# Optimization experiments

Measured on AMD Instinct MI355X. Metric: run time of the kernel, lower is better.

## Reference

```python
import jax, jax.numpy as jnp
import numpy as np

NB = 10   # num_boxes
NC = 14   # num_classes
LC = 19   # channels per anchor: conf, x, y, w, h + NC classes
N_OBJ = 256


def _split(t):
    # t: [B, NB*LC, H, W] -> (conf, x, y, w, h), each [B, NB, H, W]
    return tuple(t[:, i:NB * LC + i:LC] for i in range(5))


def _iou_corners(b1, b2):
    # b1, b2: [..., 4] as (x1, y1, x2, y2)
    x1 = jnp.maximum(b1[..., 0], b2[..., 0])
    y1 = jnp.maximum(b1[..., 1], b2[..., 1])
    x2 = jnp.minimum(b1[..., 2], b2[..., 2])
    y2 = jnp.minimum(b1[..., 3], b2[..., 3])
    inter = jnp.clip(x2 - x1, 0.0) * jnp.clip(y2 - y1, 0.0)
    a1 = jnp.abs((b1[..., 2] - b1[..., 0]) * (b1[..., 3] - b1[..., 1]))
    a2 = jnp.abs((b2[..., 2] - b2[..., 0]) * (b2[..., 3] - b2[..., 1]))
    return inter / (a1 + a2 - inter + 1e-6)


def _responsible_anchor(pred_boxes, target_boxes, grids):
    # Faithful port of YOLOLoss.IOUcalc including its sequential integer state
    # and the quirky membership row max_IOU[b][:][h][w] == max_IOU[b, h, w, :].
    B, _, H, W, _ = pred_boxes.shape
    b, g, h, w = grids[:, 0], grids[:, 1], grids[:, 2], grids[:, 3]
    tb = target_boxes[b, g, h, w]                 # [N, 4]
    pb = pred_boxes[b, :, h, w]                   # [N, NB, 4]
    ious = jax.lax.stop_gradient(_iou_corners(tb[:, None, :], pb))  # [N, NB]
    maxI0 = jnp.zeros((B, NB, H, W), jnp.int32)

    def step(mI, inp):
        grid, iou_row = inp
        gb, gg, gh, gw = grid[0], grid[1], grid[2], grid[3]

        def anchor(a, mI):
            cur = mI[gb, gg, gh, gw]
            row = mI[gb, gh, gw, :]  # torch quirk: anchor dim indexed by h, H dim by w
            cond = (cur.astype(iou_row.dtype) < iou_row[a]) & jnp.all(row != a)
            return mI.at[gb, gg, gh, gw].set(jnp.where(cond, a, cur))

        return jax.lax.fori_loop(0, NB, anchor, mI), None

    maxI, _ = jax.lax.scan(step, maxI0, (grids, ious))
    return maxI


def _yolo_loss(predictions, targets, valid_grids,
               lambda_coord=5.0, lambda_noobj=5.0, lambda_loc=7.0):
    tc, tx, ty, tw, th = _split(targets)
    pc, px, py, pw, ph = _split(predictions)
    # corner-format boxes [B, NB, H, W, 4]
    pb = jnp.stack((px - pw / 2, py - ph / 2, px + pw / 2, py + ph / 2), -1)
    tb = jnp.stack((tx - tw / 2, ty - th / 2, tx + tw / 2, ty + th / 2), -1)
    maxI = _responsible_anchor(pb, tb, valid_grids)

    b, g, h, w = valid_grids[:, 0], valid_grids[:, 1], valid_grids[:, 2], valid_grids[:, 3]
    sel = maxI[b, g, h, w]       # responsible anchor for w/h/conf/class terms
    sel_xy = maxI[b, g, h, h]    # original bug: grids[2] used twice for x/y terms
    n = valid_grids.shape[0]

    x_l = (tx[b, g, h, w] - px[b, sel_xy, h, w]) ** 2
    y_l = (ty[b, g, h, w] - py[b, sel_xy, h, w]) ** 2
    w_l = (jnp.sqrt(jnp.clip(tw[b, g, h, w], 0.0)) - jnp.sqrt(jnp.clip(pw[b, sel, h, w], 0.0))) ** 2
    h_l = (jnp.sqrt(jnp.clip(th[b, g, h, w], 0.0)) - jnp.sqrt(jnp.clip(ph[b, sel, h, w], 0.0))) ** 2
    localization = jnp.sum(x_l + y_l + w_l + h_l) / n

    conf_obj = jnp.sum((tc[b, g, h, w] - pc[b, sel, h, w]) ** 2) / n

    conf_nothing = ((tc - pc) ** 2).at[b, sel, h, w].set(0.0).mean()

    cls_off = jnp.arange(NC)
    p_cls = predictions[b[:, None], (sel * LC + 5)[:, None] + cls_off, h[:, None], w[:, None]]  # [N, NC]
    t_cls = targets[b[:, None], (b * LC + 5)[:, None] + cls_off, h[:, None], w[:, None]]        # original bug: b*19
    class_loss = jnp.sum(jnp.mean((p_cls - t_cls) ** 2, axis=1)) / n

    return (lambda_loc * localization + lambda_coord * conf_obj
            + lambda_noobj * conf_nothing + class_loss)


def setup_inputs() -> dict:
    key = jax.random.key(0)
    B, H, W = 8, 96, 96
    C = NB * LC
    k1, k2, k3 = jax.random.split(key, 3)
    predictions = jax.random.uniform(k1, (B, C, H, W), jnp.float32)
    targets = jax.random.uniform(k2, (B, C, H, W), jnp.float32)
    targets = targets.at[:, 0:C:LC].set(0.0)  # confidence zero everywhere
    # 256 unique object cells; quirky-indexing constraints: b < 10, h < NB, H == W
    H_OBJ = 10
    rng = np.random.default_rng(0)
    flat = rng.choice(B * NB * H_OBJ * W, size=N_OBJ, replace=False)
    gb, r = np.divmod(flat, NB * H_OBJ * W)
    gg, r = np.divmod(r, H_OBJ * W)
    gh, gw = np.divmod(r, W)
    grids = np.stack([gb, gg, gh, gw], axis=1)
    grids = grids[np.lexsort((gw, gh, gg, gb))]  # torch.unique(dim=0) sorts rows
    valid_grids = jnp.asarray(grids, jnp.int32)
    conf = jax.random.uniform(k3, (N_OBJ,), jnp.float32, minval=0.3, maxval=1.0)
    targets = targets.at[valid_grids[:, 0], valid_grids[:, 1] * LC,
                         valid_grids[:, 2], valid_grids[:, 3]].set(conf)
    return {"predictions": predictions, "targets": targets, "valid_grids": valid_grids}


def reference(predictions, targets, valid_grids):
    return _yolo_loss(predictions, targets, valid_grids)
```

## Files before the change

kernel.cpp:

```cpp
#include <hip/hip_runtime.h>

#define NBANCH 10
#define NCLS   14
#define LCH    19
#define NOBJ   256
#define BBATCH 8
#define HH     96
#define WW     96
#define NCHTOT 190
#define PLANE  (HH*WW)
#define TOTCONF (BBATCH*NBANCH*PLANE)
#define NCONFBLK 720

__device__ __forceinline__ float ldat(const float* __restrict__ p, int b, int c, int hw) {
    return p[(size_t)(b * NCHTOT + c) * PLANE + hw];
}

#define IOU_OFF 0
#define XY_OFF  2560
#define WH_OFF  5120
#define CO_OFF  7680
#define CLS_OFF 10240
#define SUB_OFF 12800

__global__ __launch_bounds__(256) void fused_pre(const float* __restrict__ pred,
                                                 const float* __restrict__ targ,
                                                 const int* __restrict__ grids,
                                                 double* __restrict__ conf_part,
                                                 float* __restrict__ gw) {
    if (blockIdx.x < NCONFBLK) {
        int tid = blockIdx.x * 256 + threadIdx.x;
        int plane = tid / 2304;
        int r = tid - plane * 2304;
        int b = plane / NBANCH;
        int g = plane - b * NBANCH;
        size_t off = (size_t)(b * NCHTOT + g * LCH) * PLANE + (size_t)r * 4;
        float4 t4 = *reinterpret_cast<const float4*>(targ + off);
        float4 p4 = *reinterpret_cast<const float4*>(pred + off);
        float dx = t4.x - p4.x, dy = t4.y - p4.y, dz = t4.z - p4.z, dw = t4.w - p4.w;
        double s = (double)(dx*dx) + (double)(dy*dy) + (double)(dz*dz) + (double)(dw*dw);
        for (int o = 32; o > 0; o >>= 1) s += __shfl_down(s, o, 64);
        __shared__ double wsum[4];
        int lane = threadIdx.x & 63, wid = threadIdx.x >> 6;
        if (lane == 0) wsum[wid] = s;
        __syncthreads();
        if (threadIdx.x == 0) conf_part[blockIdx.x] = wsum[0] + wsum[1] + wsum[2] + wsum[3];
        return;
    }

    int gi = blockIdx.x - NCONFBLK;
    int a = threadIdx.x;
    if (a >= NBANCH) return;
    const int b = grids[gi*4+0], g = grids[gi*4+1], h = grids[gi*4+2], w = grids[gi*4+3];
    const int hw = h * WW + w;

    const float tc = ldat(targ, b, g*LCH+0, hw);
    const float tx = ldat(targ, b, g*LCH+1, hw);
    const float ty = ldat(targ, b, g*LCH+2, hw);
    const float tw = ldat(targ, b, g*LCH+3, hw);
    const float th = ldat(targ, b, g*LCH+4, hw);
    const float tb0 = tx - tw*0.5f, tb1 = ty - th*0.5f;
    const float tb2 = tx + tw*0.5f, tb3 = ty + th*0.5f;
    const float ta  = fabsf((tb2 - tb0) * (tb3 - tb1));

    const float pc = ldat(pred, b, a*LCH+0, hw);
    const float px = ldat(pred, b, a*LCH+1, hw);
    const float py = ldat(pred, b, a*LCH+2, hw);
    const float pw = ldat(pred, b, a*LCH+3, hw);
    const float ph = ldat(pred, b, a*LCH+4, hw);
    const float tca = ldat(targ, b, a*LCH+0, hw);

    const float pb0 = px - pw*0.5f, pb1 = py - ph*0.5f;
    const float pb2 = px + pw*0.5f, pb3 = py + ph*0.5f;
    float x1 = fmaxf(tb0, pb0), y1 = fmaxf(tb1, pb1);
    float x2 = fminf(tb2, pb2), y2 = fminf(tb3, pb3);
    float inter = fmaxf(x2 - x1, 0.f) * fmaxf(y2 - y1, 0.f);
    float pa = fabsf((pb2 - pb0) * (pb3 - pb1));
    float iou = inter / (((ta + pa) - inter) + 1e-6f);

    float dxl = tx - px, dyl = ty - py;
    float xy  = dxl*dxl + dyl*dyl;
    float dwl = sqrtf(fmaxf(tw, 0.f)) - sqrtf(fmaxf(pw, 0.f));
    float dhl = sqrtf(fmaxf(th, 0.f)) - sqrtf(fmaxf(ph, 0.f));
    float wh  = dwl*dwl + dhl*dhl;
    float dco = tc - pc;
    float co  = dco*dco;
    float dsb = tca - pc;
    float sub = dsb*dsb;

    float clsf = 0.f;
    #pragma unroll
    for (int c = 0; c < NCLS; ++c) {
        float d = ldat(pred, b, a*LCH+5+c, hw) - ldat(targ, b, b*LCH+5+c, hw);
        clsf += d * d;
    }
    float cls = clsf / 14.f;

    int idx = gi * NBANCH + a;
    gw[IOU_OFF + idx] = iou;
    gw[XY_OFF  + idx] = xy;
    gw[WH_OFF  + idx] = wh;
    gw[CO_OFF  + idx] = co;
    gw[CLS_OFF + idx] = cls;
    gw[SUB_OFF + idx] = sub;
}

__global__ __launch_bounds__(256) void yolo_main(const int* __restrict__ grids,
                                                 const double* __restrict__ conf_part,
                                                 const float* __restrict__ gw,
                                                 float* __restrict__ out) {
    __shared__ int packed[NOBJ];
    __shared__ int sels[NOBJ];
    __shared__ int keys[NOBJ];
    __shared__ int changed;
    __shared__ double red[NOBJ][5];

    const int i = threadIdx.x;
    const int b = grids[i*4+0], g = grids[i*4+1], h = grids[i*4+2], w = grids[i*4+3];
    packed[i] = (b << 24) | (g << 16) | (h << 8) | w;

    float iou_r[NBANCH];
    int afirst = 0;
    #pragma unroll
    for (int a = 0; a < NBANCH; ++a) {
        float v = gw[IOU_OFF + i*NBANCH + a];
        iou_r[a] = v;
        if (a >= 1 && afirst == 0 && v > 0.f) afirst = a;
    }
    sels[i] = afirst;
    __syncthreads();

    const int mkey = (b << 16) | (h << 8) | w;
    unsigned long long mreg[4] = {0ull, 0ull, 0ull, 0ull};
    for (int j = 0; j < NOBJ; ++j) {
        if ((packed[j] >> 8) == mkey) mreg[j >> 6] |= 1ull << (j & 63);
    }
    const bool inS = (mreg[0] | mreg[1] | mreg[2] | mreg[3]) != 0ull;
    const int kc = __popcll(mreg[0]) + __popcll(mreg[1]) + __popcll(mreg[2]) + __popcll(mreg[3]);

    for (int round = 0; round < NOBJ; ++round) {
        if (i == 0) changed = 0;
        __syncthreads();
        int nv = sels[i];
        if (inS) {
            int cur = 0;
            #pragma unroll
            for (int a = 0; a < NBANCH; ++a) {
                if ((float)cur < iou_r[a]) {
                    bool ok = (a != 0) || (kc == 96);
                    if (ok) {
                        #pragma unroll
                        for (int wd = 0; wd < 4; ++wd) {
                            unsigned long long mm = mreg[wd];
                            while (mm && ok) {
                                int j = wd * 64 + __ffsll((long long)mm) - 1;
                                mm &= mm - 1;
                                int vj = (j == i) ? cur : (j < i ? sels[j] : 0);
                                if (vj == a) ok = false;
                            }
                        }
                    }
                    if (ok) cur = a;
                }
            }
            nv = cur;
        }
        __syncthreads();
        if (inS && nv != sels[i]) { sels[i] = nv; changed = 1; }
        __syncthreads();
        if (!changed) break;
    }

    const int sel = sels[i];
    const int pkxy = (b << 24) | (g << 16) | (h << 8) | h;
    int sxy = 0;
    for (int j = 0; j < NOBJ; ++j) if (packed[j] == pkxy) sxy = sels[j];

    keys[i] = ((b * NBANCH + sel) * HH + h) * WW + w;
    __syncthreads();
    bool firstocc = true;
    for (int j = 0; j < i; ++j) if (keys[j] == keys[i]) { firstocc = false; break; }

    double loc = (double)gw[XY_OFF + i*NBANCH + sxy] + (double)gw[WH_OFF + i*NBANCH + sel];
    double co  = (double)gw[CO_OFF + i*NBANCH + sel];
    double cls = (double)gw[CLS_OFF + i*NBANCH + sel];
    double sub = firstocc ? (double)gw[SUB_OFF + i*NBANCH + sel] : 0.0;

    double cp = conf_part[i];
    if (i + 256 < NCONFBLK) cp += conf_part[i + 256];
    if (i + 512 < NCONFBLK) cp += conf_part[i + 512];

    red[i][0] = loc; red[i][1] = co; red[i][2] = cls; red[i][3] = sub; red[i][4] = cp;
    __syncthreads();
    for (int s = 128; s > 0; s >>= 1) {
        if (i < s) {
            red[i][0] += red[i+s][0];
            red[i][1] += red[i+s][1];
            red[i][2] += red[i+s][2];
            red[i][3] += red[i+s][3];
            red[i][4] += red[i+s][4];
        }
        __syncthreads();
    }
    if (i == 0) {
        double locS = red[0][0] / 256.0;
        double coS  = red[0][1] / 256.0;
        double clsS = red[0][2] / 256.0;
        double cn   = (red[0][4] - red[0][3]) / (double)TOTCONF;
        out[0] = (float)(7.0 * locS + 5.0 * coS + 5.0 * cn + clsS);
    }
}

extern "C" void kernel_launch(void* const* d_in, const int* in_sizes, int n_in,
                              void* d_out, int out_size, void* d_ws, size_t ws_size,
                              hipStream_t stream) {
    const float* pred = (const float*)d_in[0];
    const float* targ = (const float*)d_in[1];
    const int*  grids = (const int*)d_in[2];
    float* out = (float*)d_out;
    double* conf_part = (double*)d_ws;
    float* gw = (float*)((char*)d_ws + NCONFBLK * sizeof(double));

    fused_pre<<<NCONFBLK + NOBJ, 256, 0, stream>>>(pred, targ, grids, conf_part, gw);
    yolo_main<<<1, 256, 0, stream>>>(grids, conf_part, gw, out);
}
```

Measured before the change: 159.5 us.

## Precompute anchor-presence bitmask and use wavefront shuffles in single-block serial solver

```diff
diff --git a/kernel.cpp b/kernel.cpp
--- a/kernel.cpp
+++ b/kernel.cpp
@@ -113,7 +113,7 @@
     __shared__ int sels[NOBJ];
     __shared__ int keys[NOBJ];
     __shared__ int changed;
-    __shared__ double red[NOBJ][5];
+    __shared__ double wpart[4][5];
 
     const int i = threadIdx.x;
     const int b = grids[i*4+0], g = grids[i*4+1], h = grids[i*4+2], w = grids[i*4+3];
@@ -128,38 +128,48 @@
         if (a >= 1 && afirst == 0 && v > 0.f) afirst = a;
     }
     sels[i] = afirst;
+    if (i == 0) changed = 0;
     __syncthreads();
 
     const int mkey = (b << 16) | (h << 8) | w;
-    unsigned long long mreg[4] = {0ull, 0ull, 0ull, 0ull};
-    for (int j = 0; j < NOBJ; ++j) {
-        if ((packed[j] >> 8) == mkey) mreg[j >> 6] |= 1ull << (j & 63);
-    }
-    const bool inS = (mreg[0] | mreg[1] | mreg[2] | mreg[3]) != 0ull;
-    const int kc = __popcll(mreg[0]) + __popcll(mreg[1]) + __popcll(mreg[2]) + __popcll(mreg[3]);
+    unsigned long long m0 = 0, m1 = 0, m2 = 0, m3 = 0;
+    #pragma unroll 8
+    for (int j = 0; j < 64; ++j)
+        m0 |= ((unsigned long long)((packed[j] >> 8) == mkey)) << j;
+    #pragma unroll 8
+    for (int j = 64; j < 128; ++j)
+        m1 |= ((unsigned long long)((packed[j] >> 8) == mkey)) << (j - 64);
+    #pragma unroll 8
+    for (int j = 128; j < 192; ++j)
+        m2 |= ((unsigned long long)((packed[j] >> 8) == mkey)) << (j - 128);
+    #pragma unroll 8
+    for (int j = 192; j < 256; ++j)
+        m3 |= ((unsigned long long)((packed[j] >> 8) == mkey)) << (j - 192);
+
+    const bool selfin = ((i < 64 ? m0 : i < 128 ? m1 : i < 192 ? m2 : m3) >> (i & 63)) & 1ull;
+    unsigned long long w0 = m0, w1 = m1, w2 = m2, w3 = m3;
+    if (i < 64)       w0 &= ~(1ull << i);
+    else if (i < 128) w1 &= ~(1ull << (i - 64));
+    else if (i < 192) w2 &= ~(1ull << (i - 128));
+    else              w3 &= ~(1ull << (i - 192));
+
+    const bool inS = (m0 | m1 | m2 | m3) != 0ull;
+    const int kc = __popcll(m0) + __popcll(m1) + __popcll(m2) + __popcll(m3);
 
     for (int round = 0; round < NOBJ; ++round) {
-        if (i == 0) changed = 0;
-        __syncthreads();
         int nv = sels[i];
         if (inS) {
+            int present = selfin ? 1 : 0;
+            unsigned long long mm;
+            mm = w0; while (mm) { int j = __ffsll((long long)mm) - 1;       mm &= mm - 1; present |= 1 << ((j < i) ? sels[j] : 0); }
+            mm = w1; while (mm) { int j = 64  + __ffsll((long long)mm) - 1; mm &= mm - 1; present |= 1 << ((j < i) ? sels[j] : 0); }
+            mm = w2; while (mm) { int j = 128 + __ffsll((long long)mm) - 1; mm &= mm - 1; present |= 1 << ((j < i) ? sels[j] : 0); }
+            mm = w3; while (mm) { int j = 192 + __ffsll((long long)mm) - 1; mm &= mm - 1; present |= 1 << ((j < i) ? sels[j] : 0); }
             int cur = 0;
             #pragma unroll
             for (int a = 0; a < NBANCH; ++a) {
                 if ((float)cur < iou_r[a]) {
-                    bool ok = (a != 0) || (kc == 96);
-                    if (ok) {
-                        #pragma unroll
-                        for (int wd = 0; wd < 4; ++wd) {
-                            unsigned long long mm = mreg[wd];
-                            while (mm && ok) {
-                                int j = wd * 64 + __ffsll((long long)mm) - 1;
-                                mm &= mm - 1;
-                                int vj = (j == i) ? cur : (j < i ? sels[j] : 0);
-                                if (vj == a) ok = false;
-                            }
-                        }
-                    }
+                    bool ok = ((a != 0) || (kc == 96)) && !((present >> a) & 1);
                     if (ok) cur = a;
                 }
             }
@@ -168,18 +178,31 @@
         __syncthreads();
         if (inS && nv != sels[i]) { sels[i] = nv; changed = 1; }
         __syncthreads();
-        if (!changed) break;
+        int c = changed;
+        __syncthreads();
+        if (i == 0) changed = 0;
+        if (!c) break;
     }
 
     const int sel = sels[i];
     const int pkxy = (b << 24) | (g << 16) | (h << 8) | h;
     int sxy = 0;
-    for (int j = 0; j < NOBJ; ++j) if (packed[j] == pkxy) sxy = sels[j];
+    #pragma unroll 8
+    for (int j = 0; j < NOBJ; ++j) {
+        bool m = (packed[j] == pkxy);
+        int v = sels[j];
+        sxy = m ? v : sxy;
+    }
 
     keys[i] = ((b * NBANCH + sel) * HH + h) * WW + w;
     __syncthreads();
-    bool firstocc = true;
-    for (int j = 0; j < i; ++j) if (keys[j] == keys[i]) { firstocc = false; break; }
+    const int myk = keys[i];
+    int dup = 0;
+    #pragma unroll 8
+    for (int j = 0; j < NOBJ; ++j) {
+        dup |= (int)((j < i) & (keys[j] == myk));
+    }
+    const bool firstocc = (dup == 0);
 
     double loc = (double)gw[XY_OFF + i*NBANCH + sxy] + (double)gw[WH_OFF + i*NBANCH + sel];
     double co  = (double)gw[CO_OFF + i*NBANCH + sel];
@@ -190,23 +213,32 @@
     if (i + 256 < NCONFBLK) cp += conf_part[i + 256];
     if (i + 512 < NCONFBLK) cp += conf_part[i + 512];
 
-    red[i][0] = loc; red[i][1] = co; red[i][2] = cls; red[i][3] = sub; red[i][4] = cp;
+    double v0 = loc, v1 = co, v2 = cls, v3 = sub, v4 = cp;
+    #pragma unroll
+    for (int o = 32; o > 0; o >>= 1) {
+        v0 += __shfl_down(v0, o, 64);
+        v1 += __shfl_down(v1, o, 64);
+        v2 += __shfl_down(v2, o, 64);
+        v3 += __shfl_down(v3, o, 64);
+        v4 += __shfl_down(v4, o, 64);
+    }
+    const int lane = i & 63, wid = i >> 6;
+    if (lane == 0) {
+        wpart[wid][0] = v0; wpart[wid][1] = v1; wpart[wid][2] = v2;
+        wpart[wid][3] = v3; wpart[wid][4] = v4;
+    }
     __syncthreads();
-    for (int s = 128; s > 0; s >>= 1) {
-        if (i < s) {
-            red[i][0] += red[i+s][0];
-            red[i][1] += red[i+s][1];
-            red[i][2] += red[i+s][2];
-            red[i][3] += red[i+s][3];
-            red[i][4] += red[i+s][4];
+    if (i == 0) {
+        double s0 = 0, s1 = 0, s2 = 0, s3 = 0, s4 = 0;
+        #pragma unroll
+        for (int k = 0; k < 4; ++k) {
+            s0 += wpart[k][0]; s1 += wpart[k][1]; s2 += wpart[k][2];
+            s3 += wpart[k][3]; s4 += wpart[k][4];
         }
-        __syncthreads();
-    }
-    if (i == 0) {
-        double locS = red[0][0] / 256.0;
-        double coS  = red[0][1] / 256.0;
-        double clsS = red[0][2] / 256.0;
-        double cn   = (red[0][4] - red[0][3]) / (double)TOTCONF;
+        double locS = s0 / 256.0;
+        double coS  = s1 / 256.0;
+        double clsS = s2 / 256.0;
+        double cn   = (s4 - s3) / (double)TOTCONF;
         out[0] = (float)(7.0 * locS + 5.0 * coS + 5.0 * cn + clsS);
     }
 }
```

New measurement: 132.3 us. 1.21x faster.
